# Optimization experiments

Hardware: AMD Instinct MI355X
Metric: run time of the kernel (lower is better)

## Reference

```python
import jax, jax.numpy as jnp
import numpy as np

B, T, D, E, P = 32, 8192, 256, 16, 64  # batch, tokens, dim, num_spectral_blocks, pixels_per_patch


def setup_inputs() -> dict:
    key = jax.random.key(0)
    k1, k2, k3, k4 = jax.random.split(key, 4)
    x = jax.random.normal(k1, (B, T, D), dtype=jnp.float32)
    block_indices = jax.random.randint(k2, (B, T), 0, E)
    # per-expert Linear(dim -> pixels_per_patch): weight [E, D, P], bias [E, P]
    W = jax.random.normal(k3, (E, D, P), dtype=jnp.float32) * 0.02
    b = jax.random.normal(k4, (E, P), dtype=jnp.float32) * 0.02
    return {"x": x, "W": W, "b": b, "block_indices": block_indices}


def reference(x, W, b, block_indices):
    # Each token [b, t] is routed to expert block_indices[b, t]; that expert's
    # Linear(dim -> pixels_per_patch) produces the output row. Loop is over the
    # small fixed expert count (16), fully vectorized over tokens.
    num_experts = W.shape[0]
    out = jnp.zeros(x.shape[:2] + (W.shape[2],), dtype=x.dtype)
    for e in range(num_experts):
        y = x @ W[e] + b[e]                       # [B, T, P]
        sel = (block_indices == e)[..., None]      # [B, T, 1]
        out = jnp.where(sel, y, out)
    return out
```

## Files before the change

### kernel.cpp

```cpp
#include <hip/hip_runtime.h>

#define NT (32 * 8192)
#define DIM 256
#define NE 16
#define NP 64
#define NCH 64
#define CAPC 352

typedef short bf16x8 __attribute__((ext_vector_type(8)));
typedef float f32x4 __attribute__((ext_vector_type(4)));

__device__ __forceinline__ unsigned short f2bf(float f) {
  unsigned int u = __builtin_bit_cast(unsigned int, f);
  u += 0x7fffu + ((u >> 16) & 1u);
  return (unsigned short)(u >> 16);
}

__global__ void k_prep(const float* __restrict__ W, const int* __restrict__ idx,
                       unsigned short* __restrict__ Wt, int* __restrict__ cnt_ec,
                       int* __restrict__ bucket) {
  int t = threadIdx.x;
  if (blockIdx.x >= 64) {
    int gid = (blockIdx.x - 64) * 256 + t;
    int e = gid >> 10;
    int n = (gid >> 4) & 63;
    int k0 = (gid & 15) << 4;
    const float* src = W + e * (DIM * NP) + n;
    unsigned short* dst = Wt + ((e * NP + n) * DIM + k0);
    #pragma unroll
    for (int j = 0; j < 16; ++j) dst[j] = f2bf(src[(k0 + j) * NP]);
    return;
  }
  __shared__ int cur[NE];
  if (t < NE) cur[t] = 0;
  __syncthreads();
  int c = blockIdx.x;
  int b0 = c * 4096;
  #pragma unroll
  for (int i = 0; i < 16; ++i) {
    int tok = b0 + i * 256 + t;
    int e = idx[tok];
    int pos = atomicAdd(&cur[e], 1);
    if (pos < CAPC) bucket[(e * NCH + c) * CAPC + pos] = tok;
  }
  __syncthreads();
  if (t < NE) cnt_ec[t * NCH + c] = cur[t] < CAPC ? cur[t] : CAPC;
}

__global__ __launch_bounds__(256, 2) void k_gemm(
    const float* __restrict__ x, const unsigned short* __restrict__ Wt,
    const float* __restrict__ bvec, const int* __restrict__ cnt_ec,
    const int* __restrict__ bucket, float* __restrict__ out) {
  int e = blockIdx.x >> 6;
  int slice = blockIdx.x & 63;
  int w = threadIdx.x >> 6;
  int lane = threadIdx.x & 63;
  int cc = lane & 15, q = lane >> 4;

  int s = slice * 4 + w;
  int c = s >> 2;
  int sub = s & 3;

  int rows_ec = cnt_ec[e * NCH + c];
  int ntiles = (rows_ec + 15) >> 4;
  const int* bkt = bucket + (e * NCH + c) * CAPC;

  const unsigned short* wb = Wt + e * NP * DIM;
  bf16x8 bfr[4][8];
  #pragma unroll
  for (int nf = 0; nf < 4; ++nf) {
    int n = nf * 16 + cc;
    #pragma unroll
    for (int ks = 0; ks < 8; ++ks)
      bfr[nf][ks] = *(const bf16x8*)(wb + n * DIM + ks * 32 + q * 8);
  }
  float bias[4];
  #pragma unroll
  for (int nf = 0; nf < 4; ++nf) bias[nf] = bvec[e * NP + nf * 16 + cc];

  for (int rt = sub; rt < ntiles; rt += 4) {
    int r0 = rt << 4;
    int rows = rows_ec - r0;
    if (rows > 16) rows = 16;

    int myr = cc < rows ? cc : 0;
    int tok = bkt[r0 + myr];
    const float* xr = x + (long)tok * DIM + q * 8;

    f32x4 va[16];
    #pragma unroll
    for (int ks = 0; ks < 8; ++ks) {
      va[2 * ks]     = *(const f32x4*)(xr + ks * 32);
      va[2 * ks + 1] = *(const f32x4*)(xr + ks * 32 + 4);
    }

    f32x4 acc[4] = {{0.f,0.f,0.f,0.f},{0.f,0.f,0.f,0.f},
                    {0.f,0.f,0.f,0.f},{0.f,0.f,0.f,0.f}};
    #pragma unroll
    for (int ks = 0; ks < 8; ++ks) {
      bf16x8 a;
      #pragma unroll
      for (int j = 0; j < 4; ++j) {
        a[j]     = (short)f2bf(va[2 * ks][j]);
        a[4 + j] = (short)f2bf(va[2 * ks + 1][j]);
      }
      #pragma unroll
      for (int nf = 0; nf < 4; ++nf)
        acc[nf] = __builtin_amdgcn_mfma_f32_16x16x32_bf16(a, bfr[nf][ks], acc[nf], 0, 0, 0);
    }

    #pragma unroll
    for (int r = 0; r < 4; ++r) {
      int m = q * 4 + r;
      if (m < rows) {
        int tk = bkt[r0 + m];
        float* orow = out + (long)tk * NP + cc;
        #pragma unroll
        for (int nf = 0; nf < 4; ++nf) orow[nf * 16] = acc[nf][r] + bias[nf];
      }
    }
  }
}

extern "C" void kernel_launch(void* const* d_in, const int* in_sizes, int n_in,
                              void* d_out, int out_size, void* d_ws, size_t ws_size,
                              hipStream_t stream) {
  const float* x = (const float*)d_in[0];
  const float* W = (const float*)d_in[1];
  const float* b = (const float*)d_in[2];
  const int* idx = (const int*)d_in[3];
  float* out = (float*)d_out;

  int* ws = (int*)d_ws;
  int* cnt_ec = ws;
  int* bucket = ws + 1024;
  unsigned short* Wt = (unsigned short*)(ws + 1024 + NE * NCH * CAPC);

  k_prep<<<128, 256, 0, stream>>>(W, idx, Wt, cnt_ec, bucket);
  k_gemm<<<NE * 64, 256, 0, stream>>>(x, Wt, b, cnt_ec, bucket, out);
}
```

Measured before the change: 420.1 us.

## Stage expert weights in swizzled LDS instead of registers to raise occupancy

Each block now copies its expert's bf16 weight matrix (32 KB) into shared memory with an XOR swizzle, and reads B fragments from LDS inside the MFMA loop. Before, every lane held 128 VGPRs of weight fragments. Dropping those registers lets launch bounds rise from 2 to 4 blocks per CU, giving more waves to hide the latency of the gathered x loads. The bias is also folded into the accumulator initialisation. The cost is extra LDS reads per tile and a block-wide sync, and 32 KB of LDS per block may itself cap occupancy.

```diff
diff --git a/kernel.cpp b/kernel.cpp
--- a/kernel.cpp
+++ b/kernel.cpp
@@ -9,6 +9,7 @@
 
 typedef short bf16x8 __attribute__((ext_vector_type(8)));
 typedef float f32x4 __attribute__((ext_vector_type(4)));
+typedef int i32x4 __attribute__((ext_vector_type(4)));
 
 __device__ __forceinline__ unsigned short f2bf(float f) {
   unsigned int u = __builtin_bit_cast(unsigned int, f);
@@ -47,15 +48,41 @@
   if (t < NE) cnt_ec[t * NCH + c] = cur[t] < CAPC ? cur[t] : CAPC;
 }
 
-__global__ __launch_bounds__(256, 2) void k_gemm(
+__global__ __launch_bounds__(256, 4) void k_gemm(
     const float* __restrict__ x, const unsigned short* __restrict__ Wt,
     const float* __restrict__ bvec, const int* __restrict__ cnt_ec,
     const int* __restrict__ bucket, float* __restrict__ out) {
   int e = blockIdx.x >> 6;
   int slice = blockIdx.x & 63;
-  int w = threadIdx.x >> 6;
-  int lane = threadIdx.x & 63;
+  int tid = threadIdx.x;
+  int w = tid >> 6;
+  int lane = tid & 63;
   int cc = lane & 15, q = lane >> 4;
+
+  __shared__ __align__(16) unsigned short wlds[NP * DIM];
+
+  const unsigned short* wb = Wt + e * NP * DIM;
+  #pragma unroll
+  for (int it = 0; it < 8; ++it) {
+    int lin = (it * 256 + tid) * 16;
+    i32x4 v = *(const i32x4*)((const char*)wb + lin);
+    int sw = lin ^ (((lin >> 9) & 7) << 4);
+    *(i32x4*)((char*)wlds + sw) = v;
+  }
+
+  float bias[4];
+  #pragma unroll
+  for (int nf = 0; nf < 4; ++nf) bias[nf] = bvec[e * NP + nf * 16 + cc];
+
+  int base0[4], swz[4];
+  #pragma unroll
+  for (int nf = 0; nf < 4; ++nf) {
+    int n = nf * 16 + cc;
+    base0[nf] = (n << 9) + (q << 4);
+    swz[nf] = (n & 7) << 4;
+  }
+
+  __syncthreads();
 
   int s = slice * 4 + w;
   int c = s >> 2;
@@ -64,19 +91,6 @@
   int rows_ec = cnt_ec[e * NCH + c];
   int ntiles = (rows_ec + 15) >> 4;
   const int* bkt = bucket + (e * NCH + c) * CAPC;
-
-  const unsigned short* wb = Wt + e * NP * DIM;
-  bf16x8 bfr[4][8];
-  #pragma unroll
-  for (int nf = 0; nf < 4; ++nf) {
-    int n = nf * 16 + cc;
-    #pragma unroll
-    for (int ks = 0; ks < 8; ++ks)
-      bfr[nf][ks] = *(const bf16x8*)(wb + n * DIM + ks * 32 + q * 8);
-  }
-  float bias[4];
-  #pragma unroll
-  for (int nf = 0; nf < 4; ++nf) bias[nf] = bvec[e * NP + nf * 16 + cc];
 
   for (int rt = sub; rt < ntiles; rt += 4) {
     int r0 = rt << 4;
@@ -94,8 +108,11 @@
       va[2 * ks + 1] = *(const f32x4*)(xr + ks * 32 + 4);
     }
 
-    f32x4 acc[4] = {{0.f,0.f,0.f,0.f},{0.f,0.f,0.f,0.f},
-                    {0.f,0.f,0.f,0.f},{0.f,0.f,0.f,0.f}};
+    f32x4 acc[4];
+    #pragma unroll
+    for (int nf = 0; nf < 4; ++nf)
+      acc[nf] = (f32x4){bias[nf], bias[nf], bias[nf], bias[nf]};
+
     #pragma unroll
     for (int ks = 0; ks < 8; ++ks) {
       bf16x8 a;
@@ -105,8 +122,11 @@
         a[4 + j] = (short)f2bf(va[2 * ks + 1][j]);
       }
       #pragma unroll
-      for (int nf = 0; nf < 4; ++nf)
-        acc[nf] = __builtin_amdgcn_mfma_f32_16x16x32_bf16(a, bfr[nf][ks], acc[nf], 0, 0, 0);
+      for (int nf = 0; nf < 4; ++nf) {
+        const bf16x8 bf = *(const bf16x8*)(
+            (const char*)wlds + ((base0[nf] + (ks << 6)) ^ swz[nf]));
+        acc[nf] = __builtin_amdgcn_mfma_f32_16x16x32_bf16(a, bf, acc[nf], 0, 0, 0);
+      }
     }
 
     #pragma unroll
@@ -116,7 +136,7 @@
         int tk = bkt[r0 + m];
         float* orow = out + (long)tk * NP + cc;
         #pragma unroll
-        for (int nf = 0; nf < 4; ++nf) orow[nf * 16] = acc[nf][r] + bias[nf];
+        for (int nf = 0; nf < 4; ++nf) orow[nf * 16] = acc[nf][r];
       }
     }
   }
```

New measurement: 452.1 us. 7.6% more time.
